# Kernel tuning notes

Measured on AMD Instinct MI355X. Metric: run time of the kernel, lower is better.

Reference implementation:

```python
import jax, jax.numpy as jnp
import numpy as np

HEADS = 8


def setup_inputs() -> dict:
    key = jax.random.key(0)
    ks = jax.random.split(key, 9)
    B, C, W, H = 8, 512, 32, 32
    dk = C // HEADS
    return {
        "x": jax.random.normal(ks[0], (B, C, W, H), dtype=jnp.float32),
        "wq": jax.random.normal(ks[1], (C, C), dtype=jnp.float32) * (1.0 / np.sqrt(C)),
        "bq": jax.random.normal(ks[2], (C,), dtype=jnp.float32) * 0.02,
        "wk": jax.random.normal(ks[3], (C, C), dtype=jnp.float32) * (1.0 / np.sqrt(C)),
        "bk": jax.random.normal(ks[4], (C,), dtype=jnp.float32) * 0.02,
        "wv": jax.random.normal(ks[5], (C, C), dtype=jnp.float32) * (1.0 / np.sqrt(C)),
        "bv": jax.random.normal(ks[6], (C,), dtype=jnp.float32) * 0.02,
        "rel_h": jax.random.normal(ks[7], (1, HEADS, dk, 1, H), dtype=jnp.float32),
        "rel_w": jax.random.normal(ks[8], (1, HEADS, dk, W, 1), dtype=jnp.float32),
    }


def reference(x, wq, bq, wk, bk, wv, bv, rel_h, rel_w):
    B, C, W, H = x.shape
    dk = C // HEADS
    N = W * H

    def proj(w, b):
        # 1x1 conv == per-pixel linear map over channels
        y = jnp.einsum('bchw,oc->bohw', x, w) + b[None, :, None, None]
        return y.reshape(B, HEADS, dk, N)

    q = proj(wq, bq)  # [B, h, dk, N]
    k = proj(wk, bk)
    v = proj(wv, bv)

    # content-content: q^T k -> [B, h, N, N]
    content_content = jnp.einsum('bhdn,bhdm->bhnm', q, k)

    # content-position: (rel_h + rel_w) -> [1, h, dk, W, H] -> [h, dk, N]
    pos = (rel_h + rel_w).reshape(HEADS, dk, N)
    # matmul(pos^T, q): [h, N, dk] @ [B, h, dk, N] -> [B, h, N, N]
    content_position = jnp.einsum('hdn,bhdm->bhnm', pos, q)

    energy = content_content + content_position
    attention = jax.nn.softmax(energy, axis=-1)  # softmax over last dim

    # out = v @ attention^T : [B, h, dk, N]
    out = jnp.einsum('bhdn,bhmn->bhdm', v, attention)
    return out.reshape(B, C, W, H)
```

## Files before the change

kernel.cpp:

```cpp
#include <hip/hip_runtime.h>

#define NPIX 1024
#define CC   512
#define DK   64
#define LOG2E 1.4426950408889634f

typedef __attribute__((ext_vector_type(8)))  short s16x8;
typedef __attribute__((ext_vector_type(8)))  _Float16 f16x8;
typedef __attribute__((ext_vector_type(16))) float f32x16;

union U4 { uint4 u; s16x8 v; };
union U4H { uint4 u; f16x8 v; };

__device__ __forceinline__ ushort f2bf(float f) {
  uint u = __float_as_uint(f);
  uint r = (u + 0x7fffu + ((u >> 16) & 1u)) >> 16;
  return (ushort)r;
}
__device__ __forceinline__ float bf2f(ushort h) { return __uint_as_float(((uint)h) << 16); }
__device__ __forceinline__ ushort f2h(float f) {
  union { _Float16 h; ushort u; } c;
  c.h = (_Float16)f;
  return c.u;
}
__device__ __forceinline__ float h2f(ushort u) {
  union { ushort u; _Float16 h; } c;
  c.u = u;
  return (float)c.h;
}

__device__ __forceinline__ uint cvtpk(float a, float b) {
  uint r;
  asm("v_cvt_pk_bf16_f32 %0, %1, %2" : "=v"(r) : "v"(a), "v"(b));
  return r;
}
__device__ __forceinline__ float fmax3(float a, float b, float c) {
  float d;
  asm("v_max3_f32 %0, %1, %2, %3" : "=v"(d) : "v"(a), "v"(b), "v"(c));
  return d;
}
__device__ __forceinline__ float exp2raw(float x) {
  float r;
  asm("v_exp_f32 %0, %1" : "=v"(r) : "v"(x));
  return r;
}

__device__ __forceinline__ f32x16 mfma32(s16x8 a, s16x8 b, f32x16 c) {
  return __builtin_amdgcn_mfma_f32_32x32x16_bf16(a, b, c, 0, 0, 0);
}
__device__ __forceinline__ f32x16 mfma32h(f16x8 a, f16x8 b, f32x16 c) {
  return __builtin_amdgcn_mfma_f32_32x32x16_f16(a, b, c, 0, 0, 0);
}

__device__ __forceinline__ void gl16(const void* g, void* l) {
  __builtin_amdgcn_global_load_lds(
      (const __attribute__((address_space(1))) void*)g,
      (__attribute__((address_space(3))) void*)l, 16, 0, 0);
}

__global__ void pos_kernel(const float* __restrict__ rel_h,
                           const float* __restrict__ rel_w,
                           ushort* __restrict__ posH, ushort* __restrict__ posL) {
  int t = blockIdx.x * 256 + threadIdx.x;
  int g = t & 7;
  int n = (t >> 3) & (NPIX - 1);
  int h = t >> 13;
  int xw = n >> 5, yh = n & 31;
  ushort hbuf[8], lbuf[8];
#pragma unroll
  for (int j = 0; j < 8; ++j) {
    int d = g * 8 + j;
    float v = rel_h[(h * 64 + d) * 32 + yh] + rel_w[(h * 64 + d) * 32 + xw];
    ushort hi = f2h(v);
    hbuf[j] = hi;
    lbuf[j] = f2h(v - h2f(hi));
  }
  size_t base = ((size_t)(h * NPIX + n)) * 64 + g * 8;
  *(uint4*)&posH[base] = *(uint4*)hbuf;
  *(uint4*)&posL[base] = *(uint4*)lbuf;
}

__global__ __launch_bounds__(256) void cvt_w_kernel(
    const float* __restrict__ wq, const float* __restrict__ wk,
    const float* __restrict__ wv,
    ushort* __restrict__ Wh, ushort* __restrict__ Wl) {
  int lin8 = blockIdx.x * 256 + threadIdx.x;
  int p = lin8 >> 15;
  int o = (lin8 & 32767) >> 6;
  int co = lin8 & 63;
  const float* Wsrc = (p == 0) ? wq : (p == 1) ? wk : wv;
  const float* src = &Wsrc[o * CC + co * 8];
  float4 f0 = *(const float4*)src;
  float4 f1 = *(const float4*)(src + 4);
  float f[8] = {f0.x, f0.y, f0.z, f0.w, f1.x, f1.y, f1.z, f1.w};
  ushort h8[8], l8[8];
#pragma unroll
  for (int j = 0; j < 8; ++j) {
    ushort hi = f2bf(f[j]);
    h8[j] = hi;
    l8[j] = f2bf(f[j] - bf2f(hi));
  }
  size_t dst = ((size_t)(p * CC + o)) * CC + co * 8;
  *(uint4*)&Wh[dst] = *(uint4*)h8;
  *(uint4*)&Wl[dst] = *(uint4*)l8;
}

__global__ __launch_bounds__(256) void cvt_x_kernel(
    const float* __restrict__ x,
    ushort* __restrict__ Xh, ushort* __restrict__ Xl) {
  int t = blockIdx.x * 256 + threadIdx.x;
  int nl = t & (NPIX - 1);
  int rest = t >> 10;
  int co = rest & 63;
  int b = rest >> 6;
  ushort h8[8], l8[8];
#pragma unroll
  for (int j = 0; j < 8; ++j) {
    float v = x[(((size_t)(b * CC + co * 8 + j)) << 10) + nl];
    ushort hi = f2bf(v);
    h8[j] = hi;
    l8[j] = f2bf(v - bf2f(hi));
  }
  size_t dst = (((size_t)(b * NPIX + nl)) << 9) + co * 8;
  *(uint4*)&Xh[dst] = *(uint4*)h8;
  *(uint4*)&Xl[dst] = *(uint4*)l8;
}

__global__ __launch_bounds__(256, 2) void proj_kernel(
    const ushort* __restrict__ Xh, const ushort* __restrict__ Xl,
    const ushort* __restrict__ Wh, const ushort* __restrict__ Wl,
    const float* __restrict__ bq, const float* __restrict__ bk,
    const float* __restrict__ bv,
    ushort* __restrict__ KQh, ushort* __restrict__ KQl,
    ushort* __restrict__ Vb) {
  __shared__ __align__(16) ushort sW[128 * 128];
  __shared__ __align__(16) ushort sX[128 * 128];

  int tid = threadIdx.x;
  int lane = tid & 63;
  int w = tid >> 6;
  int col = lane & 31;
  int half = lane >> 5;
  int srow = lane >> 4;
  int sslot = lane & 15;

  int z = blockIdx.z;
  int b = z / 3, p = z % 3;
  const float* bias = (p == 0) ? bq : (p == 1) ? bk : bv;

  int n0 = blockIdx.x * 128;
  int o0 = blockIdx.y * 128;
  int wo = w >> 1;
  int wn = w & 1;

  f32x16 acc[2][2];
#pragma unroll
  for (int i = 0; i < 2; ++i)
#pragma unroll
    for (int j = 0; j < 2; ++j)
#pragma unroll
      for (int r = 0; r < 16; ++r) acc[i][j][r] = 0.f;

  const char* Abuf = (const char*)((p < 2) ? sX : sW);
  const char* Bbuf = (const char*)((p < 2) ? sW : sX);
  int wm = (p < 2) ? wn : wo;
  int wc = (p < 2) ? wo : wn;

#pragma unroll 1
  for (int c0 = 0; c0 < CC; c0 += 64) {
#pragma unroll
    for (int i = 0; i < 8; ++i) {
      int rbase = (i * 4 + w) * 4;
      int row = rbase + srow;
      int j = sslot ^ (row & 15);
      int jc = j & 7;
      const ushort* src = (j < 8 || p == 2) ? Wh : Wl;
      size_t g = ((size_t)(p * CC + o0 + row)) * CC + c0 + jc * 8;
      gl16(src + g, (char*)sW + rbase * 256);
    }
#pragma unroll
    for (int i = 0; i < 8; ++i) {
      int rbase = (i * 4 + w) * 4;
      int row = rbase + srow;
      int j = sslot ^ (row & 15);
      int jc = j & 7;
      const ushort* src = (j < 8 || p == 2) ? Xh : Xl;
      size_t g = ((size_t)(b * NPIX + n0 + row)) * CC + c0 + jc * 8;
      gl16(src + g, (char*)sX + rbase * 256);
    }
    __syncthreads();

#pragma unroll
    for (int s = 0; s < 4; ++s) {
      s16x8 ah[2], al[2], bh_[2], bl_[2];
#pragma unroll
      for (int mt = 0; mt < 2; ++mt) {
        int row = wm * 64 + mt * 32 + col;
        int sh = ((s * 2 + half) ^ (row & 15)) << 4;
        ah[mt] = *(const s16x8*)(Abuf + row * 256 + sh);
        if (p < 2) {
          int sl = ((8 + s * 2 + half) ^ (row & 15)) << 4;
          al[mt] = *(const s16x8*)(Abuf + row * 256 + sl);
        }
      }
#pragma unroll
      for (int ct = 0; ct < 2; ++ct) {
        int row = wc * 64 + ct * 32 + col;
        int sh = ((s * 2 + half) ^ (row & 15)) << 4;
        bh_[ct] = *(const s16x8*)(Bbuf + row * 256 + sh);
        if (p < 2) {
          int sl = ((8 + s * 2 + half) ^ (row & 15)) << 4;
          bl_[ct] = *(const s16x8*)(Bbuf + row * 256 + sl);
        }
      }
#pragma unroll
      for (int mt = 0; mt < 2; ++mt)
#pragma unroll
        for (int ct = 0; ct < 2; ++ct) {
          acc[mt][ct] = mfma32(ah[mt], bh_[ct], acc[mt][ct]);
          if (p < 2) {
            acc[mt][ct] = mfma32(ah[mt], bl_[ct], acc[mt][ct]);
            acc[mt][ct] = mfma32(al[mt], bh_[ct], acc[mt][ct]);
          }
        }
    }
    __syncthreads();
  }

  if (p < 2) {
    float qscale = (p == 0) ? LOG2E : 1.0f;
#pragma unroll
    for (int ct = 0; ct < 2; ++ct) {
      int o = o0 + wo * 64 + ct * 32 + col;
      int bh = b * 8 + (o >> 6);
      int kk = ((p == 0) ? 64 : 0) + (o & 63);
      float bias_v = bias[o];
#pragma unroll
      for (int mt = 0; mt < 2; ++mt) {
        int nbase = n0 + wn * 64 + mt * 32;
#pragma unroll
        for (int r = 0; r < 16; ++r) {
          int n = nbase + (r & 3) + 8 * (r >> 2) + 4 * half;
          float v = (acc[mt][ct][r] + bias_v) * qscale;
          ushort hi = f2h(v);
          size_t addr = (((size_t)bh << 10) + n) * 128 + kk;
          KQh[addr] = hi;
          if (p == 0) KQl[addr] = f2h(v - h2f(hi));
        }
      }
    }
  } else {
#pragma unroll
    for (int ct = 0; ct < 2; ++ct) {
      int n = n0 + wn * 64 + ct * 32 + col;
#pragma unroll
      for (int mt = 0; mt < 2; ++mt) {
        int obase = o0 + wo * 64 + mt * 32;
#pragma unroll
        for (int r = 0; r < 16; ++r) {
          int o = obase + (r & 3) + 8 * (r >> 2) + 4 * half;
          int bh = b * 8 + (o >> 6);
          int d = o & 63;
          float v = acc[mt][ct][r] + bias[o];
          Vb[(((size_t)(bh * 64 + d)) << 10) + n] = f2bf(v);
        }
      }
    }
  }
}

__global__ __launch_bounds__(256, 2) void attn_kernel(
    const ushort* __restrict__ KQh, const ushort* __restrict__ KQl,
    const ushort* __restrict__ posH, const ushort* __restrict__ posL,
    const ushort* __restrict__ Vb, float* __restrict__ out) {
  __shared__ __align__(16) ushort sKh[128 * 128];
  __shared__ __align__(16) ushort sV[64 * 128];

  int tid = threadIdx.x;
  int lane = tid & 63;
  int w = tid >> 6;

  int bid = blockIdx.x;
  int wg = (bid & 7) * 64 + (bid >> 3);
  int bh = wg >> 3;
  int qb = wg & 7;
  int h = bh & 7;

  int col = lane & 31;
  int half = lane >> 5;
  int q0 = qb * 128 + w * 32;
  int q = q0 + col;

  uint4 bqh[8], bql[8];
  {
    const ushort* rowQh = KQh + ((size_t)bh * NPIX + q) * 128;
    const ushort* rowQl = KQl + ((size_t)bh * NPIX + q) * 128;
#pragma unroll
    for (int s = 0; s < 4; ++s) {
      int off = 64 + s * 16 + half * 8;
      bqh[s] = *(const uint4*)(rowQh + off);
      bql[s] = *(const uint4*)(rowQl + off);
    }
    const ushort* rowPh = posH + ((size_t)(h * NPIX + q)) * 64;
    const ushort* rowPl = posL + ((size_t)(h * NPIX + q)) * 64;
#pragma unroll
    for (int s = 4; s < 8; ++s) {
      int off = (s - 4) * 16 + half * 8;
      bqh[s] = *(const uint4*)(rowPh + off);
      bql[s] = *(const uint4*)(rowPl + off);
    }
  }

  f32x16 oacc[2];
#pragma unroll
  for (int t = 0; t < 2; ++t)
#pragma unroll
    for (int r = 0; r < 16; ++r) oacc[t][r] = 0.f;
  float m_ = -1e30f, l_ = 0.f;

  int srow = lane >> 4;
  int sslot = lane & 15;

#pragma unroll 1
  for (int k0 = 0; k0 < NPIX; k0 += 128) {
#pragma unroll
    for (int i = 0; i < 8; ++i) {
      int row = w * 32 + i * 4 + srow;
      size_t goff = ((size_t)bh * NPIX + k0 + row) * 128 + ((sslot ^ (row & 15)) << 3);
      char* ldst = (char*)sKh + (w * 32 + i * 4) * 256;
      gl16(KQh + goff, ldst);
    }
#pragma unroll
    for (int i = 0; i < 4; ++i) {
      int d = w * 16 + i * 4 + srow;
      size_t goff = ((size_t)(bh * 64 + d)) * NPIX + k0 + ((sslot ^ (d & 15)) << 3);
      char* ldst = (char*)sV + (w * 16 + i * 4) * 256;
      gl16(Vb + goff, ldst);
    }
    __syncthreads();

    f32x16 sa[4];
#pragma unroll
    for (int t = 0; t < 4; ++t)
#pragma unroll
      for (int r = 0; r < 16; ++r) sa[t][r] = 0.f;

    __builtin_amdgcn_s_setprio(1);
#pragma unroll
    for (int s = 0; s < 8; ++s) {
      U4H ubh, ubl;
      ubh.u = bqh[s];
      ubl.u = bql[s];
#pragma unroll
      for (int t = 0; t < 4; ++t) {
        int row = t * 32 + col;
        int slot = ((s * 2 + half) ^ (row & 15)) << 4;
        const f16x8 ah = *(const f16x8*)((const char*)sKh + row * 256 + slot);
        sa[t] = mfma32h(ah, ubh.v, sa[t]);
        sa[t] = mfma32h(ah, ubl.v, sa[t]);
      }
    }
    __builtin_amdgcn_s_setprio(0);

    float mx = -1e30f;
#pragma unroll
    for (int t = 0; t < 4; ++t)
#pragma unroll
      for (int r = 0; r < 16; r += 2) mx = fmax3(mx, sa[t][r], sa[t][r + 1]);
    mx = fmaxf(mx, __shfl_xor(mx, 32));
    if (!__all(mx - m_ <= 11.54f)) {
      float mn = fmaxf(m_, mx);
      float sc = exp2raw(m_ - mn);
      l_ *= sc;
#pragma unroll
      for (int t = 0; t < 2; ++t)
#pragma unroll
        for (int r = 0; r < 16; ++r) oacc[t][r] *= sc;
      m_ = mn;
    }
    float ssum = 0.f;
#pragma unroll
    for (int t = 0; t < 4; ++t)
#pragma unroll
      for (int r = 0; r < 16; ++r) {
        float pv = exp2raw(sa[t][r] - m_);
        sa[t][r] = pv;
        ssum += pv;
      }
    ssum += __shfl_xor(ssum, 32);
    l_ += ssum;

#pragma unroll
    for (int t = 0; t < 4; ++t) {
      uint ua[4], ub[4], xa[4], xb[4];
#pragma unroll
      for (int g = 0; g < 4; ++g) {
        ua[g] = cvtpk(sa[t][4 * g + 0], sa[t][4 * g + 1]);
        ub[g] = cvtpk(sa[t][4 * g + 2], sa[t][4 * g + 3]);
      }
#pragma unroll
      for (int g = 0; g < 4; ++g) {
        xa[g] = __shfl_xor(ua[g], 32);
        xb[g] = __shfl_xor(ub[g], 32);
      }
      __builtin_amdgcn_s_setprio(1);
#pragma unroll
      for (int st = 0; st < 2; ++st) {
        int g = st * 2 + half;
        U4 pf;
        if (half == 0) {
          pf.u.x = ua[g]; pf.u.y = ub[g]; pf.u.z = xa[g]; pf.u.w = xb[g];
        } else {
          pf.u.x = xa[g]; pf.u.y = xb[g]; pf.u.z = ua[g]; pf.u.w = ub[g];
        }
#pragma unroll
        for (int dt = 0; dt < 2; ++dt) {
          int d = dt * 32 + col;
          int slot = ((t * 4 + st * 2 + half) ^ (d & 15)) << 4;
          const s16x8 vf = *(const s16x8*)((const char*)sV + d * 256 + slot);
          oacc[dt] = mfma32(vf, pf.v, oacc[dt]);
        }
      }
      __builtin_amdgcn_s_setprio(0);
    }
    __syncthreads();
  }

  float inv = 1.0f / l_;
#pragma unroll
  for (int dt = 0; dt < 2; ++dt)
#pragma unroll
    for (int r = 0; r < 16; ++r) {
      int d = dt * 32 + (r & 3) + 8 * (r >> 2) + 4 * half;
      out[((size_t)(bh * 64 + d) << 10) + q] = oacc[dt][r] * inv;
    }
}

extern "C" void kernel_launch(void* const* d_in, const int* in_sizes, int n_in,
                              void* d_out, int out_size, void* d_ws, size_t ws_size,
                              hipStream_t stream) {
  const float* x     = (const float*)d_in[0];
  const float* wq    = (const float*)d_in[1];
  const float* bq    = (const float*)d_in[2];
  const float* wk    = (const float*)d_in[3];
  const float* bk    = (const float*)d_in[4];
  const float* wv    = (const float*)d_in[5];
  const float* bv    = (const float*)d_in[6];
  const float* rel_h = (const float*)d_in[7];
  const float* rel_w = (const float*)d_in[8];
  float* out = (float*)d_out;

  const size_t MB = 1024 * 1024;
  char* ws = (char*)d_ws;
  ushort* KQh  = (ushort*)(ws);
  ushort* KQl  = (ushort*)(ws + 16 * MB);
  ushort* Vb   = (ushort*)(ws + 32 * MB);
  ushort* posH = (ushort*)(ws + 40 * MB);
  ushort* posL = (ushort*)(ws + 41 * MB);
  ushort* Xh   = (ushort*)(ws + 42 * MB);
  ushort* Xl   = (ushort*)(ws + 50 * MB);
  ushort* Wh   = (ushort*)(ws + 58 * MB);
  ushort* Wl   = (ushort*)(ws + 58 * MB + 1572864);

  pos_kernel<<<dim3(256), dim3(256), 0, stream>>>(rel_h, rel_w, posH, posL);
  cvt_w_kernel<<<dim3(384), dim3(256), 0, stream>>>(wq, wk, wv, Wh, Wl);
  cvt_x_kernel<<<dim3(2048), dim3(256), 0, stream>>>(x, Xh, Xl);
  proj_kernel<<<dim3(8, 4, 24), dim3(256), 0, stream>>>(
      Xh, Xl, Wh, Wl, bq, bk, bv, KQh, KQl, Vb);
  attn_kernel<<<dim3(512), dim3(256), 0, stream>>>(KQh, KQl, posH, posL, Vb, out);
}
```

Before: 118.6 us.

## Switch projection to fp16 with single-term X and split-fp16 scaled weights

The projection now converts X to a single fp16 term instead of a bf16 hi/lo pair. Weights are pre-scaled by 64 and split into fp16 hi/lo, with the scale removed in the epilogue. Q/K projection drops from three MFMAs per step to two, the X low-part buffer and its global traffic are gone, and the X shared tile is halved so occupancy can rise to 3 blocks. Dropping the X residual loses some input precision (fp16 has a 10-bit mantissa), and large x values could overflow fp16 range.

```diff
diff --git a/kernel.cpp b/kernel.cpp
--- a/kernel.cpp
+++ b/kernel.cpp
@@ -96,9 +96,10 @@
   ushort h8[8], l8[8];
 #pragma unroll
   for (int j = 0; j < 8; ++j) {
-    ushort hi = f2bf(f[j]);
+    float sv = f[j] * 64.0f;
+    ushort hi = f2h(sv);
     h8[j] = hi;
-    l8[j] = f2bf(f[j] - bf2f(hi));
+    l8[j] = f2h(sv - h2f(hi));
   }
   size_t dst = ((size_t)(p * CC + o)) * CC + co * 8;
   *(uint4*)&Wh[dst] = *(uint4*)h8;
@@ -106,35 +107,31 @@
 }
 
 __global__ __launch_bounds__(256) void cvt_x_kernel(
-    const float* __restrict__ x,
-    ushort* __restrict__ Xh, ushort* __restrict__ Xl) {
+    const float* __restrict__ x, ushort* __restrict__ Xh) {
   int t = blockIdx.x * 256 + threadIdx.x;
   int nl = t & (NPIX - 1);
   int rest = t >> 10;
   int co = rest & 63;
   int b = rest >> 6;
-  ushort h8[8], l8[8];
+  ushort h8[8];
 #pragma unroll
   for (int j = 0; j < 8; ++j) {
     float v = x[(((size_t)(b * CC + co * 8 + j)) << 10) + nl];
-    ushort hi = f2bf(v);
-    h8[j] = hi;
-    l8[j] = f2bf(v - bf2f(hi));
+    h8[j] = f2h(v);
   }
   size_t dst = (((size_t)(b * NPIX + nl)) << 9) + co * 8;
   *(uint4*)&Xh[dst] = *(uint4*)h8;
-  *(uint4*)&Xl[dst] = *(uint4*)l8;
-}
-
-__global__ __launch_bounds__(256, 2) void proj_kernel(
-    const ushort* __restrict__ Xh, const ushort* __restrict__ Xl,
-    const ushort* __restrict__ Wh, const ushort* __restrict__ Wl,
+}
+
+__global__ __launch_bounds__(256, 3) void proj_kernel(
+    const ushort* __restrict__ Xh, const ushort* __restrict__ Wh,
+    const ushort* __restrict__ Wl,
     const float* __restrict__ bq, const float* __restrict__ bk,
     const float* __restrict__ bv,
     ushort* __restrict__ KQh, ushort* __restrict__ KQl,
     ushort* __restrict__ Vb) {
   __shared__ __align__(16) ushort sW[128 * 128];
-  __shared__ __align__(16) ushort sX[128 * 128];
+  __shared__ __align__(16) ushort sX[128 * 64];
 
   int tid = threadIdx.x;
   int lane = tid & 63;
@@ -160,11 +157,6 @@
     for (int j = 0; j < 2; ++j)
 #pragma unroll
       for (int r = 0; r < 16; ++r) acc[i][j][r] = 0.f;
-
-  const char* Abuf = (const char*)((p < 2) ? sX : sW);
-  const char* Bbuf = (const char*)((p < 2) ? sW : sX);
-  int wm = (p < 2) ? wn : wo;
-  int wc = (p < 2) ? wo : wn;
 
 #pragma unroll 1
   for (int c0 = 0; c0 < CC; c0 += 64) {
@@ -179,54 +171,65 @@
       gl16(src + g, (char*)sW + rbase * 256);
     }
 #pragma unroll
-    for (int i = 0; i < 8; ++i) {
-      int rbase = (i * 4 + w) * 4;
-      int row = rbase + srow;
-      int j = sslot ^ (row & 15);
-      int jc = j & 7;
-      const ushort* src = (j < 8 || p == 2) ? Xh : Xl;
+    for (int i = 0; i < 4; ++i) {
+      int rbase = i * 32 + w * 8;
+      int row = rbase + (lane >> 3);
+      int jc = (lane & 7) ^ (row & 7);
       size_t g = ((size_t)(b * NPIX + n0 + row)) * CC + c0 + jc * 8;
-      gl16(src + g, (char*)sX + rbase * 256);
+      gl16(Xh + g, (char*)sX + rbase * 128);
     }
     __syncthreads();
 
 #pragma unroll
     for (int s = 0; s < 4; ++s) {
-      s16x8 ah[2], al[2], bh_[2], bl_[2];
-#pragma unroll
-      for (int mt = 0; mt < 2; ++mt) {
-        int row = wm * 64 + mt * 32 + col;
-        int sh = ((s * 2 + half) ^ (row & 15)) << 4;
-        ah[mt] = *(const s16x8*)(Abuf + row * 256 + sh);
-        if (p < 2) {
+      if (p < 2) {
+        f16x8 xa[2], wh_[2], wl_[2];
+#pragma unroll
+        for (int mt = 0; mt < 2; ++mt) {
+          int row = wn * 64 + mt * 32 + col;
+          int slot = ((s * 2 + half) ^ (row & 7)) << 4;
+          xa[mt] = *(const f16x8*)((const char*)sX + row * 128 + slot);
+        }
+#pragma unroll
+        for (int ct = 0; ct < 2; ++ct) {
+          int row = wo * 64 + ct * 32 + col;
+          int sh = ((s * 2 + half) ^ (row & 15)) << 4;
           int sl = ((8 + s * 2 + half) ^ (row & 15)) << 4;
-          al[mt] = *(const s16x8*)(Abuf + row * 256 + sl);
-        }
-      }
-#pragma unroll
-      for (int ct = 0; ct < 2; ++ct) {
-        int row = wc * 64 + ct * 32 + col;
-        int sh = ((s * 2 + half) ^ (row & 15)) << 4;
-        bh_[ct] = *(const s16x8*)(Bbuf + row * 256 + sh);
-        if (p < 2) {
-          int sl = ((8 + s * 2 + half) ^ (row & 15)) << 4;
-          bl_[ct] = *(const s16x8*)(Bbuf + row * 256 + sl);
-        }
-      }
-#pragma unroll
-      for (int mt = 0; mt < 2; ++mt)
+          wh_[ct] = *(const f16x8*)((const char*)sW + row * 256 + sh);
+          wl_[ct] = *(const f16x8*)((const char*)sW + row * 256 + sl);
+        }
+#pragma unroll
+        for (int mt = 0; mt < 2; ++mt)
+#pragma unroll
+          for (int ct = 0; ct < 2; ++ct) {
+            acc[mt][ct] = mfma32h(xa[mt], wh_[ct], acc[mt][ct]);
+            acc[mt][ct] = mfma32h(xa[mt], wl_[ct], acc[mt][ct]);
+          }
+      } else {
+        f16x8 wa[2], xb[2];
+#pragma unroll
+        for (int mt = 0; mt < 2; ++mt) {
+          int row = wo * 64 + mt * 32 + col;
+          int sh = ((s * 2 + half) ^ (row & 15)) << 4;
+          wa[mt] = *(const f16x8*)((const char*)sW + row * 256 + sh);
+        }
 #pragma unroll
         for (int ct = 0; ct < 2; ++ct) {
-          acc[mt][ct] = mfma32(ah[mt], bh_[ct], acc[mt][ct]);
-          if (p < 2) {
-            acc[mt][ct] = mfma32(ah[mt], bl_[ct], acc[mt][ct]);
-            acc[mt][ct] = mfma32(al[mt], bh_[ct], acc[mt][ct]);
-          }
-        }
+          int row = wn * 64 + ct * 32 + col;
+          int slot = ((s * 2 + half) ^ (row & 7)) << 4;
+          xb[ct] = *(const f16x8*)((const char*)sX + row * 128 + slot);
+        }
+#pragma unroll
+        for (int mt = 0; mt < 2; ++mt)
+#pragma unroll
+          for (int ct = 0; ct < 2; ++ct)
+            acc[mt][ct] = mfma32h(wa[mt], xb[ct], acc[mt][ct]);
+      }
     }
     __syncthreads();
   }
 
+  const float INV64 = 0.015625f;
   if (p < 2) {
     float qscale = (p == 0) ? LOG2E : 1.0f;
 #pragma unroll
@@ -241,7 +244,7 @@
 #pragma unroll
         for (int r = 0; r < 16; ++r) {
           int n = nbase + (r & 3) + 8 * (r >> 2) + 4 * half;
-          float v = (acc[mt][ct][r] + bias_v) * qscale;
+          float v = (acc[mt][ct][r] * INV64 + bias_v) * qscale;
           ushort hi = f2h(v);
           size_t addr = (((size_t)bh << 10) + n) * 128 + kk;
           KQh[addr] = hi;
@@ -261,7 +264,7 @@
           int o = obase + (r & 3) + 8 * (r >> 2) + 4 * half;
           int bh = b * 8 + (o >> 6);
           int d = o & 63;
-          float v = acc[mt][ct][r] + bias[o];
+          float v = acc[mt][ct][r] * INV64 + bias[o];
           Vb[(((size_t)(bh * 64 + d)) << 10) + n] = f2bf(v);
         }
       }
@@ -458,14 +461,13 @@
   ushort* posH = (ushort*)(ws + 40 * MB);
   ushort* posL = (ushort*)(ws + 41 * MB);
   ushort* Xh   = (ushort*)(ws + 42 * MB);
-  ushort* Xl   = (ushort*)(ws + 50 * MB);
-  ushort* Wh   = (ushort*)(ws + 58 * MB);
-  ushort* Wl   = (ushort*)(ws + 58 * MB + 1572864);
+  ushort* Wh   = (ushort*)(ws + 50 * MB);
+  ushort* Wl   = (ushort*)(ws + 50 * MB + 1572864);
 
   pos_kernel<<<dim3(256), dim3(256), 0, stream>>>(rel_h, rel_w, posH, posL);
   cvt_w_kernel<<<dim3(384), dim3(256), 0, stream>>>(wq, wk, wv, Wh, Wl);
-  cvt_x_kernel<<<dim3(2048), dim3(256), 0, stream>>>(x, Xh, Xl);
+  cvt_x_kernel<<<dim3(2048), dim3(256), 0, stream>>>(x, Xh);
   proj_kernel<<<dim3(8, 4, 24), dim3(256), 0, stream>>>(
-      Xh, Xl, Wh, Wl, bq, bk, bv, KQh, KQl, Vb);
+      Xh, Wh, Wl, bq, bk, bv, KQh, KQl, Vb);
   attn_kernel<<<dim3(512), dim3(256), 0, stream>>>(KQh, KQl, posH, posL, Vb, out);
 }
```

Measured after the change: 156.5 us. 31.9% more time.
